# Performance work log

Hardware: AMD Instinct MI355X
Metric: run time of the kernel (lower is better)

The kernel has to match this reference:

```python
import jax, jax.numpy as jnp
import numpy as np

B = 8192
D = 32
K = 8
H0 = 256
H1 = 256
PER = 3 * K + 1  # 25 params per dim
SCALE = 10.0
RMIN, RMAX = -SCALE / 2.0, SCALE / 2.0
MIN_BW = 1e-3; MIN_BH = 1e-3; MIN_KS = 1e-3
CUR_STEPS = 10000.0; CUR_START = 0.0
DX_MB = 1e-4   # distrax min_bin_size default
DX_MS = 1e-4   # distrax min_knot_slope default
DX_OFF = float(np.log(np.expm1(1.0 - DX_MS)))  # so softplus(0+off)+ms == 1


def _masks():
    deg_in = np.arange(1, D + 1)
    hd0 = np.arange(H0) % (D - 1) + 1
    hd1 = np.arange(H1) % (D - 1) + 1
    m0 = (hd0[:, None] >= deg_in[None, :]).astype(np.float32).T      # (D, H0)
    m1 = (hd1[:, None] >= hd0[None, :]).astype(np.float32).T        # (H0, H1)
    out_mask = (deg_in[:, None] > hd1[None, :]).astype(np.float32)  # (D, H1)
    per_mask = np.repeat(out_mask, PER, axis=0)                      # (D*PER, H1)
    return jnp.asarray(m0), jnp.asarray(m1), jnp.asarray(per_mask)

M0, M1, PER_MASK = _masks()


def made(y, W0, b0, W1, b1, W_out, b_out):
    h = jax.nn.gelu(y @ (W0 * M0) + b0)
    h = jax.nn.gelu(h @ (W1 * M1) + b1)
    proj = h @ (W_out.T * PER_MASK.T) + b_out  # (B, D*PER)
    return proj.reshape(y.shape[0], D, PER)


def _g(a, idx):
    return jnp.take_along_axis(a, idx[..., None], axis=-1)[..., 0]


def _knots(p, training_step):
    # module-level processing (rqs_from_params) ...
    w_raw, h_raw, s_raw = p[..., :K], p[..., K:2 * K], p[..., 2 * K:]
    lw = jax.nn.softmax(w_raw, axis=-1) * SCALE * (1.0 - K * MIN_BW) + MIN_BW
    lh = jax.nn.softmax(h_raw, axis=-1) * SCALE * (1.0 - K * MIN_BH) + MIN_BH
    ls = jax.nn.softplus(s_raw) + MIN_KS
    alpha = jnp.clip((jnp.asarray(training_step, jnp.float32) - CUR_START) / CUR_STEPS, 0.0, 1.0)
    bw = (1.0 - alpha) * (SCALE / K) + alpha * lw
    bh = (1.0 - alpha) * (SCALE / K) + alpha * lh
    sl = (1.0 - alpha) * 1.0 + alpha * ls
    bw = bw / jnp.sum(bw, axis=-1, keepdims=True) * SCALE
    bh = bh / jnp.sum(bh, axis=-1, keepdims=True) * SCALE
    # ... followed by distrax.RationalQuadraticSpline internal normalization
    widths = jax.nn.softmax(bw, axis=-1) * (SCALE - K * DX_MB) + DX_MB
    heights = jax.nn.softmax(bh, axis=-1) * (SCALE - K * DX_MB) + DX_MB
    slopes = jax.nn.softplus(sl + DX_OFF) + DX_MS  # (..., K+1)
    zpad = jnp.zeros_like(widths[..., :1])
    xp = RMIN + jnp.concatenate([zpad, jnp.cumsum(widths, axis=-1)], axis=-1)
    yp = RMIN + jnp.concatenate([zpad, jnp.cumsum(heights, axis=-1)], axis=-1)
    return xp, yp, widths, heights, slopes


def spline_fwd(p, x, training_step):
    xp, yp, w, h, d = _knots(p, training_step)
    inr = (x >= RMIN) & (x <= RMAX)
    xc = jnp.clip(x, RMIN, RMAX)
    idx = jnp.clip(jnp.sum((xc[..., None] >= xp[..., :-1]), axis=-1) - 1, 0, K - 1)
    xk, yk = _g(xp, idx), _g(yp, idx)
    wk, hk = _g(w, idx), _g(h, idx)
    dk, dk1 = _g(d, idx), _g(d, idx + 1)
    s = hk / wk
    xi = (xc - xk) / wk
    z1 = xi * (1.0 - xi)
    den = s + (dk1 + dk - 2.0 * s) * z1
    y = yk + hk * (s * xi * xi + dk * z1) / den
    ld = 2.0 * jnp.log(s) + jnp.log(dk1 * xi * xi + 2.0 * s * z1 + dk * (1.0 - xi) ** 2) - 2.0 * jnp.log(den)
    return jnp.where(inr, y, x), jnp.where(inr, ld, 0.0)


def spline_inv(p, y, training_step):
    xp, yp, w, h, d = _knots(p, training_step)
    inr = (y >= RMIN) & (y <= RMAX)
    yc = jnp.clip(y, RMIN, RMAX)
    idx = jnp.clip(jnp.sum((yc[..., None] >= yp[..., :-1]), axis=-1) - 1, 0, K - 1)
    xk, yk = _g(xp, idx), _g(yp, idx)
    wk, hk = _g(w, idx), _g(h, idx)
    dk, dk1 = _g(d, idx), _g(d, idx + 1)
    s = hk / wk
    t = yc - yk
    coef = dk1 + dk - 2.0 * s
    a = hk * (s - dk) + t * coef
    b = hk * dk - t * coef
    c = -s * t
    xi = 2.0 * c / (-b - jnp.sqrt(b * b - 4.0 * a * c))
    x = xi * wk + xk
    z1 = xi * (1.0 - xi)
    den = s + coef * z1
    ld = -(2.0 * jnp.log(s) + jnp.log(dk1 * xi * xi + 2.0 * s * z1 + dk * (1.0 - xi) ** 2) - 2.0 * jnp.log(den))
    return jnp.where(inr, x, y), jnp.where(inr, ld, 0.0)


def setup_inputs() -> dict:
    ks = jax.random.split(jax.random.key(0), 4)
    sd = lambda k, shp, fan: jax.random.normal(k, shp, jnp.float32) / np.sqrt(fan).astype(np.float32)
    return {
        "x": jax.random.normal(ks[0], (B, D), jnp.float32) * 1.5,
        "W0": sd(ks[1], (D, H0), D),
        "b0": jnp.zeros((H0,), jnp.float32),
        "W1": sd(ks[2], (H0, H1), H0),
        "b1": jnp.zeros((H1,), jnp.float32),
        "W_out": sd(ks[3], (D * PER, H1), H1),
        "b_out": jnp.zeros((D * PER,), jnp.float32),
        "forward": 0,
        "training_step": 10000,
    }


def reference(x, W0, b0, W1, b1, W_out, b_out, forward, training_step):
    if forward:
        p = made(x, W0, b0, W1, b1, W_out, b_out)  # (B, D, PER)
        z, ld = spline_fwd(p, x, training_step)
        return z, jnp.sum(ld, axis=1)
    z = x

    def body(carry, i):
        x_so, ldj = carry
        p = made(x_so, W0, b0, W1, b1, W_out, b_out)
        p_i = jax.lax.dynamic_index_in_dim(p, i, axis=1, keepdims=False)  # (B, PER)
        z_i = jax.lax.dynamic_index_in_dim(z, i, axis=1, keepdims=False)  # (B,)
        x_i, ld = spline_inv(p_i, z_i, training_step)
        return (x_so.at[:, i].set(x_i), ldj + ld), None

    init = (jnp.zeros_like(z), jnp.zeros((z.shape[0],), z.dtype))
    (x_fin, ldj), _ = jax.lax.scan(body, init, jnp.arange(D))
    return x_fin, ldj
```

## Files before the change

kernel.cpp:

```cpp
#include <hip/hip_runtime.h>

typedef _Float16 f16x8 __attribute__((ext_vector_type(8)));
typedef float f32x4 __attribute__((ext_vector_type(4)));

#define NB 8192
#define DD 32
#define PER 25
#define STRH 272

#define FENCE_C() do { asm volatile("" ::: "memory"); \
                       __builtin_amdgcn_sched_barrier(0); } while (0)
#define FENCE_HW() do { asm volatile("s_waitcnt lgkmcnt(0)" ::: "memory"); \
                        __builtin_amdgcn_sched_barrier(0); } while (0)

__device__ __forceinline__ float rcp_f(float x) { return __builtin_amdgcn_rcpf(x); }
__device__ __forceinline__ float gelu_f(float x) {
    float a = -1.5957691216057308f * (x + 0.044715f * x * x * x);
    return x * rcp_f(1.0f + __expf(a));
}
__device__ __forceinline__ float softplus_f(float x) {
    return (x > 20.0f) ? x : __logf(1.0f + __expf(x));
}
__device__ __forceinline__ int cntf(int d) {
    return (d <= 0) ? 0 : ((d <= 8) ? 9 * d : 72 + 8 * (d - 8));
}
__device__ __forceinline__ int porig(int u) {
    int d = (u < 72) ? (u / 9 + 1) : ((u - 72) / 8 + 9);
    int s = (u < 72) ? (u % 9) : ((u - 72) % 8);
    return s * 31 + (d - 1);
}

template<int CTRL>
__device__ __forceinline__ float qperm(float v) {
    return __int_as_float(__builtin_amdgcn_update_dpp(
        0, __float_as_int(v), CTRL, 0xF, 0xF, true));
}
__device__ __forceinline__ float qsum2(float v) {
    v += qperm<0xB1>(v);
    v += qperm<0x4E>(v);
    return v;
}
__device__ __forceinline__ float qmax2(float v) {
    v = fmaxf(v, qperm<0xB1>(v));
    v = fmaxf(v, qperm<0x4E>(v));
    return v;
}
__device__ __forceinline__ float qscan(float v, int p) {
    float t = qperm<0x90>(v);
    float c = v + ((p >= 1) ? t : 0.0f);
    float t2 = qperm<0x44>(c);
    return c + ((p >= 2) ? t2 : 0.0f);
}
__device__ __forceinline__ float sel4(float r0, float r1, float r2, float r3, int m) {
    float lo = (m & 1) ? r1 : r0;
    float hi = (m & 1) ? r3 : r2;
    return (m & 2) ? hi : lo;
}

__global__ void prep_kernel(const float* __restrict__ W0, const float* __restrict__ b0,
                            const float* __restrict__ W1, const float* __restrict__ b1,
                            const float* __restrict__ Wout, const float* __restrict__ bout,
                            _Float16* __restrict__ W0F, _Float16* __restrict__ W1F,
                            _Float16* __restrict__ WoutF,
                            float* __restrict__ b0F, float* __restrict__ b1F,
                            float* __restrict__ boutF)
{
    const int total = 16384 + 131072 + 262144 + 512 + 512 + 1024;
    for (int e = blockIdx.x * blockDim.x + threadIdx.x; e < total;
         e += gridDim.x * blockDim.x) {
        if (e < 16384) {
            int i = e >> 9, r = e & 511, lane = r >> 3, j = r & 7;
            int c = lane & 15, k = ((lane >> 4) << 3) + j;
            int nn = cntf(i) - cntf(i - 1);
            float v = 0.0f;
            if (c < nn && k < i) v = W0[k * 256 + (c * 31 + i - 1)];
            W0F[e] = (_Float16)v;
        } else if (e < 16384 + 131072) {
            int m = e - 16384;
            int i = m >> 12, r = m & 4095, kt = r >> 9, r2 = r & 511;
            int lane = r2 >> 3, j = r2 & 7;
            int c = lane & 15, kpos = kt * 32 + ((lane >> 4) << 3) + j;
            int nn = cntf(i) - cntf(i - 1), chi = cntf(i);
            float v = 0.0f;
            if (c < nn && kpos < chi) v = W1[porig(kpos) * 256 + (c * 31 + i - 1)];
            W1F[m] = (_Float16)v;
        } else if (e < 16384 + 131072 + 262144) {
            int m = e - (16384 + 131072);
            int i = m >> 13, r = m & 8191, ct = r >> 12, r2 = r & 4095;
            int kt = r2 >> 9, r3 = r2 & 511, lane = r3 >> 3, j = r3 & 7;
            int par = ct * 16 + (lane & 15), kpos = kt * 32 + ((lane >> 4) << 3) + j;
            int chi = cntf(i);
            float v = 0.0f;
            if (par < 25 && kpos < chi) v = Wout[(i * 25 + par) * 256 + porig(kpos)];
            WoutF[m] = (_Float16)v;
        } else if (e < 409600 + 512) {
            int m = e - 409600;
            int i = m >> 4, c = m & 15;
            int nn = cntf(i) - cntf(i - 1);
            b0F[m] = (c < nn) ? b0[c * 31 + i - 1] : 0.0f;
        } else if (e < 410112 + 512) {
            int m = e - 410112;
            int i = m >> 4, c = m & 15;
            int nn = cntf(i) - cntf(i - 1);
            b1F[m] = (c < nn) ? b1[c * 31 + i - 1] : 0.0f;
        } else {
            int m = e - 410624;
            int i = m >> 5, c = m & 31;
            boutF[m] = (c < 25) ? bout[i * 25 + c] : 0.0f;
        }
    }
}

__global__ __launch_bounds__(64, 1) void inv_kernel(
    const float* __restrict__ z, const float* __restrict__ W0raw,
    const _Float16* __restrict__ W0F, const _Float16* __restrict__ W1F,
    const _Float16* __restrict__ WoutF,
    const float* __restrict__ b0F, const float* __restrict__ b1F,
    const float* __restrict__ boutF,
    const int* __restrict__ tstep_p,
    float* __restrict__ xout, float* __restrict__ ldj)
{
    __shared__ float zs[16 * 33];
    __shared__ float xs[16 * 33];
    __shared__ float ps[16 * 33];
    __shared__ __align__(16) _Float16 h0L[16 * STRH];
    __shared__ __align__(16) _Float16 h1L[16 * STRH];

    const int l = threadIdx.x;
    const int c16 = l & 15;
    const int g = l >> 4;
    const int row0 = blockIdx.x * 16;

    for (int idx = l; idx < 512; idx += 64) {
        int r = idx >> 5, c = idx & 31;
        zs[r * 33 + c] = z[row0 * 32 + idx];
    }
    {
        unsigned int* p0 = (unsigned int*)h0L;
        unsigned int* p1 = (unsigned int*)h1L;
        for (int idx = l; idx < 16 * STRH / 2; idx += 64) { p0[idx] = 0u; p1[idx] = 0u; }
    }

    f16x8 xfrag;
#pragma unroll
    for (int j = 0; j < 8; ++j) xfrag[j] = (_Float16)0.0f;

    const float alpha = fminf(fmaxf(((float)(*tstep_p)) / 10000.0f, 0.0f), 1.0f);
    const float oma = 1.0f - alpha;
    const float dxoff = logf(expm1f(0.9999f));

    float ldreg = 0.0f;

    f16x8 wa2[2];
    float b0v2[2], b1v2[2], boA2[2], boB2[2];
    float w0i2[2];
    f32x4 accA;
    f32x4 xi4;
    wa2[0] = *(const f16x8*)&W0F[l * 8];
    b0v2[0] = b0F[c16];
    b1v2[0] = b1F[c16];
    boA2[0] = boutF[c16];
    boB2[0] = boutF[16 + c16];
    w0i2[0] = 0.0f;
#pragma unroll
    for (int q = 0; q < 4; ++q) { accA[q] = 0.0f; xi4[q] = 0.0f; }

    FENCE_HW();

#pragma unroll 1
    for (int ib = 0; ib < DD; ib += 2) {
#pragma unroll
        for (int ph = 0; ph < 2; ++ph) {
            const int i = ib + ph;
            const int clo = cntf(i - 1);
            const int chi = cntf(i);
            const int nn = chi - clo;
            const int ip = (i + 1 < DD) ? (i + 1) : (DD - 1);

            const float zi = zs[(l >> 2) * 33 + i];

            wa2[ph ^ 1] = *(const f16x8*)&W0F[ip * 512 + l * 8];
            b0v2[ph ^ 1] = b0F[ip * 16 + c16];
            b1v2[ph ^ 1] = b1F[ip * 16 + c16];
            boA2[ph ^ 1] = boutF[ip * 32 + c16];
            boB2[ph ^ 1] = boutF[ip * 32 + 16 + c16];
            {
                int widx = c16 * 31 + i;
                widx = (widx > 255) ? 255 : widx;
                w0i2[ph ^ 1] = W0raw[i * 256 + widx];
            }

            f16x8 wb_r[8], wc_r[2][8];
#pragma unroll
            for (int kt = 0; kt < 8; ++kt)
                wb_r[kt] = *(const f16x8*)&W1F[i * 4096 + kt * 512 + l * 8];
#pragma unroll
            for (int ct = 0; ct < 2; ++ct)
#pragma unroll
                for (int kt = 0; kt < 8; ++kt)
                    wc_r[ct][kt] = *(const f16x8*)&WoutF[i * 8192 + ct * 4096 + kt * 512 + l * 8];

            if (nn > 0) {
                float bb = b0v2[ph];
                float w0i = w0i2[ph];
                if (c16 < nn) {
                    const int col = clo + c16;
#pragma unroll
                    for (int q = 0; q < 4; ++q) {
                        float v = accA[q] + xi4[q] * w0i + bb;
                        int row = g * 4 + q;
                        int phys = (col & ~31) | ((col & 31) ^ (8 * (row & 3)));
                        h0L[row * STRH + phys] = (_Float16)gelu_f(v);
                    }
                }
            }
            FENCE_HW();

            if (nn > 0) {
                const int fbase = c16 * STRH + ((g ^ (c16 & 3)) << 3);
                f32x4 acc;
#pragma unroll
                for (int q = 0; q < 4; ++q) acc[q] = 0.0f;
#pragma unroll
                for (int kt = 0; kt < 8; ++kt) {
                    if (kt * 32 < chi) {
                        f16x8 af = *(const f16x8*)&h0L[fbase + kt * 32];
                        acc = __builtin_amdgcn_mfma_f32_16x16x32_f16(af, wb_r[kt], acc, 0, 0, 0);
                    }
                }
                float bb = b1v2[ph];
                if (c16 < nn) {
                    const int col = clo + c16;
#pragma unroll
                    for (int q = 0; q < 4; ++q) {
                        int row = g * 4 + q;
                        int phys = (col & ~31) | ((col & 31) ^ (8 * (row & 3)));
                        h1L[row * STRH + phys] = (_Float16)gelu_f(acc[q] + bb);
                    }
                }
            }
            FENCE_HW();

            {
                const int fbase = c16 * STRH + ((g ^ (c16 & 3)) << 3);
                f32x4 acc0, acc1;
#pragma unroll
                for (int q = 0; q < 4; ++q) { acc0[q] = 0.0f; acc1[q] = 0.0f; }
#pragma unroll
                for (int kt = 0; kt < 8; ++kt) {
                    if (kt * 32 < chi) {
                        f16x8 af = *(const f16x8*)&h1L[fbase + kt * 32];
                        acc0 = __builtin_amdgcn_mfma_f32_16x16x32_f16(af, wc_r[0][kt], acc0, 0, 0, 0);
                        acc1 = __builtin_amdgcn_mfma_f32_16x16x32_f16(af, wc_r[1][kt], acc1, 0, 0, 0);
                    }
                }
                float boA = boA2[ph], boB = boB2[ph];
#pragma unroll
                for (int q = 0; q < 4; ++q)
                    ps[(g * 4 + q) * 33 + c16] = acc0[q] + boA;
                if (16 + c16 < 25) {
#pragma unroll
                    for (int q = 0; q < 4; ++q)
                        ps[(g * 4 + q) * 33 + 16 + c16] = acc1[q] + boB;
                }
            }

            {
                f32x4 zz;
#pragma unroll
                for (int q = 0; q < 4; ++q) zz[q] = 0.0f;
                accA = __builtin_amdgcn_mfma_f32_16x16x32_f16(xfrag, wa2[ph ^ 1], zz, 0, 0, 0);
            }
            FENCE_HW();

            float xv_sel;
            {
                const int r4 = l >> 2;
                const int p  = l & 3;

                const float* bp = &ps[r4 * 33];
                float w_a = bp[p],      w_b = bp[4 + p];
                float h_a = bp[8 + p],  h_b = bp[12 + p];
                float d_a = bp[16 + p], d_b = bp[20 + p], d_cin = bp[24];

                float m_w = qmax2(fmaxf(w_a, w_b));
                float ewa = __expf(w_a - m_w), ewb = __expf(w_b - m_w);
                float rsw = rcp_f(qsum2(ewa + ewb));
                float bwa = oma * 1.25f + alpha * (ewa * rsw * 9.92f + 0.001f);
                float bwb = oma * 1.25f + alpha * (ewb * rsw * 9.92f + 0.001f);
                float scw = 10.0f * rcp_f(qsum2(bwa + bwb));
                bwa *= scw; bwb *= scw;
                float e2wa = __expf(bwa), e2wb = __expf(bwb);
                float rs2w = rcp_f(qsum2(e2wa + e2wb));
                float wdt_a = e2wa * rs2w * 9.9992f + 1e-4f;
                float wdt_b = e2wb * rs2w * 9.9992f + 1e-4f;

                float m_h = qmax2(fmaxf(h_a, h_b));
                float eha = __expf(h_a - m_h), ehb = __expf(h_b - m_h);
                float rsh = rcp_f(qsum2(eha + ehb));
                float bha = oma * 1.25f + alpha * (eha * rsh * 9.92f + 0.001f);
                float bhb = oma * 1.25f + alpha * (ehb * rsh * 9.92f + 0.001f);
                float sch = 10.0f * rcp_f(qsum2(bha + bhb));
                bha *= sch; bhb *= sch;
                float e2ha = __expf(bha), e2hb = __expf(bhb);
                float rs2h = rcp_f(qsum2(e2ha + e2hb));
                float hgt_a = e2ha * rs2h * 9.9992f + 1e-4f;
                float hgt_b = e2hb * rs2h * 9.9992f + 1e-4f;

                float dsl_a = softplus_f(oma + alpha * (softplus_f(d_a) + 0.001f) + dxoff) + 1e-4f;
                float dsl_b = softplus_f(oma + alpha * (softplus_f(d_b) + 0.001f) + dxoff) + 1e-4f;
                float dsl_c = softplus_f(oma + alpha * (softplus_f(d_cin) + 0.001f) + dxoff) + 1e-4f;

                float ca  = qscan(wdt_a, p);
                float cb  = qscan(wdt_b, p) + qperm<0xFF>(ca);
                float cha = qscan(hgt_a, p);
                float chb = qscan(hgt_b, p) + qperm<0xFF>(cha);

                float wdA1 = qperm<0xB1>(wdt_a), wdA2 = qperm<0x4E>(wdt_a), wdA3 = qperm<0x1B>(wdt_a);
                float wdB1 = qperm<0xB1>(wdt_b), wdB2 = qperm<0x4E>(wdt_b), wdB3 = qperm<0x1B>(wdt_b);
                float hgA1 = qperm<0xB1>(hgt_a), hgA2 = qperm<0x4E>(hgt_a), hgA3 = qperm<0x1B>(hgt_a);
                float hgB1 = qperm<0xB1>(hgt_b), hgB2 = qperm<0x4E>(hgt_b), hgB3 = qperm<0x1B>(hgt_b);
                float dsA1 = qperm<0xB1>(dsl_a), dsA2 = qperm<0x4E>(dsl_a), dsA3 = qperm<0x1B>(dsl_a);
                float dsB1 = qperm<0xB1>(dsl_b), dsB2 = qperm<0x4E>(dsl_b), dsB3 = qperm<0x1B>(dsl_b);
                float caA1 = qperm<0xB1>(ca),    caA2 = qperm<0x4E>(ca),    caA3 = qperm<0x1B>(ca);
                float caB1 = qperm<0xB1>(cb),    caB2 = qperm<0x4E>(cb),    caB3 = qperm<0x1B>(cb);
                float chA1 = qperm<0xB1>(cha),   chA2 = qperm<0x4E>(cha),   chA3 = qperm<0x1B>(cha);
                float chB1 = qperm<0xB1>(chb),   chB2 = qperm<0x4E>(chb),   chB3 = qperm<0x1B>(chb);

                const bool inr = (zi >= -5.0f) && (zi <= 5.0f);
                const float yc = fminf(fmaxf(zi, -5.0f), 5.0f);

                float ch7 = qperm<0xFF>(chb);
                int cnt = 0;
                cnt += (yc >= cha  - 5.0f); cnt += (yc >= chA1 - 5.0f);
                cnt += (yc >= chA2 - 5.0f); cnt += (yc >= chA3 - 5.0f);
                cnt += (yc >= chb  - 5.0f); cnt += (yc >= chB1 - 5.0f);
                cnt += (yc >= chB2 - 5.0f); cnt += (yc >= chB3 - 5.0f);
                int idx = cnt - ((yc >= ch7 - 5.0f) ? 1 : 0);

                int mA = (idx & 3) ^ p;
                bool hiH = (idx >= 4);
                float wk = hiH ? sel4(wdt_b, wdB1, wdB2, wdB3, mA)
                               : sel4(wdt_a, wdA1, wdA2, wdA3, mA);
                float hk = hiH ? sel4(hgt_b, hgB1, hgB2, hgB3, mA)
                               : sel4(hgt_a, hgA1, hgA2, hgA3, mA);
                float dk = hiH ? sel4(dsl_b, dsB1, dsB2, dsB3, mA)
                               : sel4(dsl_a, dsA1, dsA2, dsA3, mA);
                int j1 = idx + 1;
                int mJ = (j1 & 3) ^ p;
                float d1A = sel4(dsl_a, dsA1, dsA2, dsA3, mJ);
                float d1B = sel4(dsl_b, dsB1, dsB2, dsB3, mJ);
                float dk1 = (j1 < 4) ? d1A : ((j1 < 8) ? d1B : dsl_c);
                int im1 = idx - 1;
                int mM = (im1 & 3) ^ p;
                float cwm = (im1 < 4) ? sel4(ca, caA1, caA2, caA3, mM)
                                      : sel4(cb, caB1, caB2, caB3, mM);
                float chm = (im1 < 4) ? sel4(cha, chA1, chA2, chA3, mM)
                                      : sel4(chb, chB1, chB2, chB3, mM);
                float xk = (idx == 0) ? -5.0f : (cwm - 5.0f);
                float yk = (idx == 0) ? -5.0f : (chm - 5.0f);

                float s_ = hk * rcp_f(wk);
                float tt = yc - yk;
                float coef = dk1 + dk - 2.0f * s_;
                float aa = hk * (s_ - dk) + tt * coef;
                float bb = hk * dk - tt * coef;
                float cc = -s_ * tt;
                float disc = bb * bb - 4.0f * aa * cc;
                float xi = 2.0f * cc * rcp_f(-bb - __builtin_amdgcn_sqrtf(disc));
                float xv = xi * wk + xk;
                float z1 = xi * (1.0f - xi);
                float den = s_ + coef * z1;
                float omxi = 1.0f - xi;
                float num = dk1 * xi * xi + 2.0f * s_ * z1 + dk * omxi * omxi;
                float ld = __logf(den * den * rcp_f(s_ * s_ * num));

                xv_sel = inr ? xv : zi;
                ldreg += inr ? ld : 0.0f;
                if (p == 0) xs[(l >> 2) * 33 + i] = xv_sel;
            }

            {
#pragma unroll
                for (int q = 0; q < 4; ++q)
                    xi4[q] = __shfl(xv_sel, (g * 4 + q) << 2);
                float xnew = __shfl(xv_sel, (l & 15) << 2);
                if (g == (i >> 3)) {
#pragma unroll
                    for (int j = 0; j < 8; ++j)
                        if (j == (i & 7)) xfrag[j] = (_Float16)xnew;
                }
            }
            FENCE_C();
        }
    }

    FENCE_HW();
    for (int idx = l; idx < 512; idx += 64) {
        int r = idx >> 5, c = idx & 31;
        xout[row0 * 32 + idx] = xs[r * 33 + c];
    }
    if ((l & 3) == 0) ldj[row0 + (l >> 2)] = ldreg;
}

extern "C" void kernel_launch(void* const* d_in, const int* in_sizes, int n_in,
                              void* d_out, int out_size, void* d_ws, size_t ws_size,
                              hipStream_t stream)
{
    const float* z    = (const float*)d_in[0];
    const float* W0   = (const float*)d_in[1];
    const float* b0   = (const float*)d_in[2];
    const float* W1   = (const float*)d_in[3];
    const float* b1   = (const float*)d_in[4];
    const float* Wout = (const float*)d_in[5];
    const float* bout = (const float*)d_in[6];
    const int* tstep  = (const int*)d_in[8];

    float* out  = (float*)d_out;
    float* xout = out;
    float* ldj  = out + NB * DD;

    _Float16* W0F   = (_Float16*)d_ws;
    _Float16* W1F   = W0F + 16384;
    _Float16* WoutF = W1F + 131072;
    float* b0F  = (float*)(WoutF + 262144);
    float* b1F  = b0F + 512;
    float* boutF = b1F + 512;

    prep_kernel<<<1608, 256, 0, stream>>>(W0, b0, W1, b1, Wout, bout,
                                          W0F, W1F, WoutF, b0F, b1F, boutF);
    inv_kernel<<<NB / 16, 64, 0, stream>>>(z, W0, W0F, W1F, WoutF, b0F, b1F, boutF,
                                           tstep, xout, ldj);
}
```

Before: 82.85 us.

## Prefetch next-step MADE weights and precompute frozen K-tiles early

Moves the per-step W1/Wout register loads to the end of the previous step so they overlap with the spline computation. It also starts the next step's hidden-layer MFMA accumulation early, over K-tiles of h0/h1 that are already final, so each step only has to multiply the newly written tiles. This shortens the sequential critical path of the autoregressive inverse loop. In exchange it keeps more weight and accumulator registers live across the spline stage, which may raise register pressure and lower occupancy.

```diff
diff --git a/kernel.cpp b/kernel.cpp
--- a/kernel.cpp
+++ b/kernel.cpp
@@ -148,6 +148,7 @@
     const float alpha = fminf(fmaxf(((float)(*tstep_p)) / 10000.0f, 0.0f), 1.0f);
     const float oma = 1.0f - alpha;
     const float dxoff = logf(expm1f(0.9999f));
+    const int fbase = c16 * STRH + ((g ^ (c16 & 3)) << 3);
 
     float ldreg = 0.0f;
 
@@ -155,7 +156,9 @@
     float b0v2[2], b1v2[2], boA2[2], boB2[2];
     float w0i2[2];
     f32x4 accA;
+    f32x4 accB, accC0, accC1;
     f32x4 xi4;
+    f16x8 wb_r[8], wc_r[2][8];
     wa2[0] = *(const f16x8*)&W0F[l * 8];
     b0v2[0] = b0F[c16];
     b1v2[0] = b1F[c16];
@@ -163,7 +166,18 @@
     boB2[0] = boutF[16 + c16];
     w0i2[0] = 0.0f;
 #pragma unroll
-    for (int q = 0; q < 4; ++q) { accA[q] = 0.0f; xi4[q] = 0.0f; }
+    for (int q = 0; q < 4; ++q) {
+        accA[q] = 0.0f; xi4[q] = 0.0f;
+        accB[q] = 0.0f; accC0[q] = 0.0f; accC1[q] = 0.0f;
+    }
+#pragma unroll
+    for (int kt = 0; kt < 8; ++kt)
+        wb_r[kt] = *(const f16x8*)&W1F[kt * 512 + l * 8];
+#pragma unroll
+    for (int ct = 0; ct < 2; ++ct)
+#pragma unroll
+        for (int kt = 0; kt < 8; ++kt)
+            wc_r[ct][kt] = *(const f16x8*)&WoutF[ct * 4096 + kt * 512 + l * 8];
 
     FENCE_HW();
 
@@ -175,6 +189,7 @@
             const int clo = cntf(i - 1);
             const int chi = cntf(i);
             const int nn = chi - clo;
+            const int nfz = clo >> 5;
             const int ip = (i + 1 < DD) ? (i + 1) : (DD - 1);
 
             const float zi = zs[(l >> 2) * 33 + i];
@@ -189,16 +204,6 @@
                 widx = (widx > 255) ? 255 : widx;
                 w0i2[ph ^ 1] = W0raw[i * 256 + widx];
             }
-
-            f16x8 wb_r[8], wc_r[2][8];
-#pragma unroll
-            for (int kt = 0; kt < 8; ++kt)
-                wb_r[kt] = *(const f16x8*)&W1F[i * 4096 + kt * 512 + l * 8];
-#pragma unroll
-            for (int ct = 0; ct < 2; ++ct)
-#pragma unroll
-                for (int kt = 0; kt < 8; ++kt)
-                    wc_r[ct][kt] = *(const f16x8*)&WoutF[i * 8192 + ct * 4096 + kt * 512 + l * 8];
 
             if (nn > 0) {
                 float bb = b0v2[ph];
@@ -217,15 +222,11 @@
             FENCE_HW();
 
             if (nn > 0) {
-                const int fbase = c16 * STRH + ((g ^ (c16 & 3)) << 3);
-                f32x4 acc;
-#pragma unroll
-                for (int q = 0; q < 4; ++q) acc[q] = 0.0f;
 #pragma unroll
                 for (int kt = 0; kt < 8; ++kt) {
-                    if (kt * 32 < chi) {
+                    if (kt >= nfz && kt * 32 < chi) {
                         f16x8 af = *(const f16x8*)&h0L[fbase + kt * 32];
-                        acc = __builtin_amdgcn_mfma_f32_16x16x32_f16(af, wb_r[kt], acc, 0, 0, 0);
+                        accB = __builtin_amdgcn_mfma_f32_16x16x32_f16(af, wb_r[kt], accB, 0, 0, 0);
                     }
                 }
                 float bb = b1v2[ph];
@@ -235,33 +236,29 @@
                     for (int q = 0; q < 4; ++q) {
                         int row = g * 4 + q;
                         int phys = (col & ~31) | ((col & 31) ^ (8 * (row & 3)));
-                        h1L[row * STRH + phys] = (_Float16)gelu_f(acc[q] + bb);
+                        h1L[row * STRH + phys] = (_Float16)gelu_f(accB[q] + bb);
                     }
                 }
             }
             FENCE_HW();
 
             {
-                const int fbase = c16 * STRH + ((g ^ (c16 & 3)) << 3);
-                f32x4 acc0, acc1;
-#pragma unroll
-                for (int q = 0; q < 4; ++q) { acc0[q] = 0.0f; acc1[q] = 0.0f; }
 #pragma unroll
                 for (int kt = 0; kt < 8; ++kt) {
-                    if (kt * 32 < chi) {
+                    if (kt >= nfz && kt * 32 < chi) {
                         f16x8 af = *(const f16x8*)&h1L[fbase + kt * 32];
-                        acc0 = __builtin_amdgcn_mfma_f32_16x16x32_f16(af, wc_r[0][kt], acc0, 0, 0, 0);
-                        acc1 = __builtin_amdgcn_mfma_f32_16x16x32_f16(af, wc_r[1][kt], acc1, 0, 0, 0);
+                        accC0 = __builtin_amdgcn_mfma_f32_16x16x32_f16(af, wc_r[0][kt], accC0, 0, 0, 0);
+                        accC1 = __builtin_amdgcn_mfma_f32_16x16x32_f16(af, wc_r[1][kt], accC1, 0, 0, 0);
                     }
                 }
                 float boA = boA2[ph], boB = boB2[ph];
 #pragma unroll
                 for (int q = 0; q < 4; ++q)
-                    ps[(g * 4 + q) * 33 + c16] = acc0[q] + boA;
+                    ps[(g * 4 + q) * 33 + c16] = accC0[q] + boA;
                 if (16 + c16 < 25) {
 #pragma unroll
                     for (int q = 0; q < 4; ++q)
-                        ps[(g * 4 + q) * 33 + 16 + c16] = acc1[q] + boB;
+                        ps[(g * 4 + q) * 33 + 16 + c16] = accC1[q] + boB;
                 }
             }
 
@@ -272,6 +269,30 @@
                 accA = __builtin_amdgcn_mfma_f32_16x16x32_f16(xfrag, wa2[ph ^ 1], zz, 0, 0, 0);
             }
             FENCE_HW();
+
+#pragma unroll
+            for (int kt = 0; kt < 8; ++kt)
+                wb_r[kt] = *(const f16x8*)&W1F[ip * 4096 + kt * 512 + l * 8];
+#pragma unroll
+            for (int ct = 0; ct < 2; ++ct)
+#pragma unroll
+                for (int kt = 0; kt < 8; ++kt)
+                    wc_r[ct][kt] = *(const f16x8*)&WoutF[ip * 8192 + ct * 4096 + kt * 512 + l * 8];
+            {
+                const int nfzN = chi >> 5;
+#pragma unroll
+                for (int q = 0; q < 4; ++q) { accB[q] = 0.0f; accC0[q] = 0.0f; accC1[q] = 0.0f; }
+#pragma unroll
+                for (int kt = 0; kt < 8; ++kt) {
+                    if (kt < nfzN) {
+                        f16x8 a0 = *(const f16x8*)&h0L[fbase + kt * 32];
+                        accB = __builtin_amdgcn_mfma_f32_16x16x32_f16(a0, wb_r[kt], accB, 0, 0, 0);
+                        f16x8 a1 = *(const f16x8*)&h1L[fbase + kt * 32];
+                        accC0 = __builtin_amdgcn_mfma_f32_16x16x32_f16(a1, wc_r[0][kt], accC0, 0, 0, 0);
+                        accC1 = __builtin_amdgcn_mfma_f32_16x16x32_f16(a1, wc_r[1][kt], accC1, 0, 0, 0);
+                    }
+                }
+            }
 
             float xv_sel;
             {
```

Measured after the change: 94.93 us. 14.6% more time.
